# Kernel tuning notes

Hardware: AMD Instinct MI355X
Metric: run time of the kernel (lower is better)

The kernel has to match this reference:

```python
import jax, jax.numpy as jnp
import numpy as np

B, C_IN, C_OUT, H, W, K, NK = 16, 256, 256, 64, 64, 3, 2
EPS = 1e-8


def setup_inputs() -> dict:
    key = jax.random.key(0)
    k1, k2, k3, k4 = jax.random.split(key, 4)
    x = jax.random.normal(k1, (B, C_IN, H, W), dtype=jnp.float32)
    mod = jax.random.normal(k2, (B, C_IN), dtype=jnp.float32)
    kernel_mod = jax.random.normal(k3, (B, NK), dtype=jnp.float32)
    # kernel bank: [num_conv_kernels, dim_out, dim_in, k, k] (kaiming-ish scale)
    weights = jax.random.normal(k4, (NK, C_OUT, C_IN, K, K), dtype=jnp.float32) / np.sqrt(C_IN * K * K)
    gamma = jnp.ones((C_OUT,), dtype=jnp.float32)
    return {"x": x, "mod": mod, "kernel_mod": kernel_mod, "weights": weights, "gamma": gamma}


def _block(x, mod, kernel_mod, weights, gamma):
    # adaptive kernel selection: softmax-mix the kernel bank per sample
    attn = jax.nn.softmax(kernel_mod, axis=-1)                       # [b, n]
    w = jnp.einsum('bn,noikl->boikl', attn, weights)                 # [b, o, i, k, k]
    # style modulation over input channels
    w = w * (mod[:, None, :, None, None] + 1.0)
    # demodulation
    denom = jnp.clip(jnp.sum(w * w, axis=(2, 3, 4), keepdims=True), EPS)
    w = w * jax.lax.rsqrt(denom)
    # per-sample conv (groups=b trick in torch) -> vmap over batch
    def conv_one(fmap, wb):
        return jax.lax.conv_general_dilated(
            fmap[None], wb, window_strides=(1, 1), padding='SAME',
            dimension_numbers=('NCHW', 'OIHW', 'NCHW'))[0]
    y = jax.vmap(conv_one)(x, w)                                     # [b, o, h, w]
    # RMSNorm over channel dim: F.normalize(x, dim=1) * gamma * sqrt(dim)
    norm = jnp.sqrt(jnp.sum(y * y, axis=1, keepdims=True))
    y = y / jnp.maximum(norm, 1e-12)
    y = y * gamma[None, :, None, None] * (gamma.shape[0] ** 0.5)
    # SiLU
    return y * jax.nn.sigmoid(y)


def reference(x, mod, kernel_mod, weights, gamma):
    return _block(x, mod, kernel_mod, weights, gamma)
```

## Files before the change

### kernel.cpp

```cpp
#include <hip/hip_runtime.h>
#include <math.h>


typedef __attribute__((ext_vector_type(8))) short short8;
typedef __attribute__((ext_vector_type(4))) float f32x4;

#define GLL16(src, dst)                                                       \
  __builtin_amdgcn_global_load_lds(                                           \
      (const __attribute__((address_space(1))) unsigned int*)(src),           \
      (__attribute__((address_space(3))) unsigned int*)(dst), 16, 0, 0)

static __device__ __forceinline__ unsigned short f2bf(float v) {
  union { float f; unsigned u; } u;
  u.f = v;
  unsigned r = u.u + 0x7FFF + ((u.u >> 16) & 1);
  return (unsigned short)(r >> 16);
}

__global__ __launch_bounds__(256) void wprep(
    const float* __restrict__ mod, const float* __restrict__ kmod,
    const float* __restrict__ weights, unsigned short* __restrict__ wq) {
  int blk = blockIdx.x;
  int b = blk >> 5, oq = blk & 31;
  int t = threadIdx.x;
  int o_l = t >> 5, its = t & 31;
  int o = oq * 8 + o_l;

  float k0 = kmod[b * 2 + 0], k1 = kmod[b * 2 + 1];
  float mx = fmaxf(k0, k1);
  float e0 = expf(k0 - mx), e1 = expf(k1 - mx);
  float ai = 1.0f / (e0 + e1);
  float a0 = e0 * ai, a1 = e1 * ai;

  float wv[9][8];
  float s = 0.0f;
  const float* w0 = &weights[((size_t)o * 256 + its * 8) * 9];
  const float* w1 = w0 + 589824;
#pragma unroll
  for (int e = 0; e < 8; ++e) {
    float f = mod[b * 256 + its * 8 + e] + 1.0f;
#pragma unroll
    for (int j = 0; j < 9; ++j) {
      float v = (a0 * w0[e * 9 + j] + a1 * w1[e * 9 + j]) * f;
      wv[j][e] = v;
      s = fmaf(v, v, s);
    }
  }

  __shared__ float red[8][32];
  __shared__ float scl[8];
  red[o_l][its] = s;
  __syncthreads();
  if (t < 8) {
    float tot = 0.0f;
#pragma unroll
    for (int k = 0; k < 32; ++k) tot += red[t][k];
    scl[t] = rsqrtf(fmaxf(tot, 1e-8f));
  }
  __syncthreads();
  float sc = scl[o_l];

  int c = its >> 1, io = its & 1;
  int ot = o >> 7, mf = (o & 127) >> 4, lm = o & 15;
  size_t cbase = ((size_t)(b * 32 + ot * 16 + c)) * 20480;
#pragma unroll
  for (int j = 0; j < 9; ++j) {
    int p = io * 10 + j;
    int sp = p >> 2, g = p & 3;
    short8 pk;
#pragma unroll
    for (int e = 0; e < 8; ++e) pk[e] = (short)f2bf(wv[j][e] * sc);
    *(short8*)(wq + cbase + sp * 4096 + mf * 512 + g * 128 + lm * 8) = pk;
  }
  {
    int c2 = t >> 4, io2 = (t >> 3) & 1, olq = t & 7;
    int o2 = oq * 8 + olq;
    int ot2 = o2 >> 7, mf2 = (o2 & 127) >> 4, lm2 = o2 & 15;
    int p2 = io2 * 10 + 9;
    int sp2 = p2 >> 2, g2 = p2 & 3;
    short8 z = {0, 0, 0, 0, 0, 0, 0, 0};
    *(short8*)(wq + ((size_t)(b * 32 + ot2 * 16 + c2)) * 20480 + sp2 * 4096 +
               mf2 * 512 + g2 * 128 + lm2 * 8) = z;
  }
}

__global__ __launch_bounds__(256) void xprep(
    const float* __restrict__ x, unsigned short* __restrict__ xq) {
  int blk = blockIdx.x;
  int rowp = blk % 66;
  int bc = blk / 66;
  int b = bc >> 4, c = bc & 15;
  int t = threadIdx.x;
  size_t obase = (size_t)blk * 1056;

  if (rowp == 0 || rowp == 65) {
    for (int idx = t; idx < 1056; idx += 256) xq[obase + idx] = 0;
    return;
  }
  __shared__ __align__(16) unsigned short xs2[1056];
  int row = rowp - 1;
  for (int idx = t; idx < 1056; idx += 256) xs2[idx] = 0;
  __syncthreads();
#pragma unroll
  for (int k = 0; k < 4; ++k) {
    int idx = t + k * 256;
    int il = idx >> 6, col = idx & 63;
    float v = x[(((size_t)b * 256 + c * 16 + il) * 64 + row) * 64 + col];
    xs2[(col + 1) * 16 + il] = f2bf(v);
  }
  __syncthreads();
  if (t < 132) {
    int S = 4 * (rowp & 7) + t;
    int fl = ((S >> 3) & 1) | (((S >> 4) & 1) << 1);
    *(short8*)(xq + obase + (size_t)(t ^ fl) * 8) = *(const short8*)&xs2[t * 8];
  }
}

__global__ __launch_bounds__(256, 1) void conv_mfma(
    const unsigned short* __restrict__ xq, const unsigned short* __restrict__ wq,
    float* __restrict__ out) {
  __shared__ __align__(16) unsigned short wsm[2][20480];
  __shared__ __align__(16) unsigned short xsm[2][10560];

  int bid = blockIdx.x;
  int xcd = bid & 7;
  int kk = bid >> 3;
  int b = xcd * 2 + (kk >> 4);
  int rem = kk & 15;
  int ot = rem >> 3;
  int rt = rem & 7;
  int r0 = rt * 8;

  int t = threadIdx.x;
  int w = t >> 6, lane = t & 63;
  int g = (t >> 4) & 3, lm = t & 15;
  int aoff = lane * 16;

  int b0_[5], b1_[5];
#pragma unroll
  for (int s = 0; s < 5; ++s) {
    int p = 4 * s + g;
    int io = (p >= 10) ? 1 : 0;
    int j = p - 10 * io;
    int jd3, jm3;
    if (j == 9) { jd3 = 0; jm3 = 0; }
    else { jd3 = (j >= 3) + (j >= 6); jm3 = j - 3 * jd3; }
    int la0 = ((2 * w + jd3) * 66 + lm + jm3) * 32 + io * 16;
    la0 ^= (((la0 >> 7) & 1) << 4) ^ (((la0 >> 8) & 1) << 5);
    b0_[s] = la0;
    int la1 = ((2 * w + 1 + jd3) * 66 + lm + jm3) * 32 + io * 16;
    la1 ^= (((la1 >> 7) & 1) << 4) ^ (((la1 >> 8) & 1) << 5);
    b1_[s] = la1;
  }

  f32x4 acc[8][8];
#pragma unroll
  for (int mf = 0; mf < 8; ++mf)
#pragma unroll
    for (int nf = 0; nf < 8; ++nf) acc[mf][nf] = (f32x4){0.f, 0.f, 0.f, 0.f};

#define WGLL(cn, nb, r)                                                         \
  {                                                                             \
    const unsigned short* s_ =                                                  \
        wq + ((size_t)(b * 32 + ot * 16 + (cn))) * 20480 + ((r) * 256 + t) * 8; \
    GLL16(s_, &wsm[nb][((r) * 256 + t) * 8]);                                   \
  }
#define XGLL(cn, nb, r)                                                          \
  {                                                                              \
    const unsigned short* s_ =                                                   \
        xq + ((size_t)((b * 16 + (cn)) * 66 + r0)) * 1056 + ((r) * 256 + t) * 8; \
    GLL16(s_, &xsm[nb][((r) * 256 + t) * 8]);                                    \
  }
#define XGLLP(cn, nb)                                                            \
  {                                                                              \
    const unsigned short* s_ =                                                   \
        xq + ((size_t)((b * 16 + (cn)) * 66 + r0)) * 1056 + (1280 + t) * 8;      \
    GLL16(s_, &xsm[nb][(1280 + t) * 8]);                                         \
  }

#define LGKM0 asm volatile("s_waitcnt lgkmcnt(0)" ::: "memory")
#define VM0 asm volatile("s_waitcnt vmcnt(0)" ::: "memory")

  WGLL(0, 0, 0); WGLL(0, 0, 1); WGLL(0, 0, 2); WGLL(0, 0, 3); WGLL(0, 0, 4);
  WGLL(0, 0, 5); WGLL(0, 0, 6); WGLL(0, 0, 7); WGLL(0, 0, 8); WGLL(0, 0, 9);
  XGLL(0, 0, 0); XGLL(0, 0, 1); XGLL(0, 0, 2); XGLL(0, 0, 3); XGLL(0, 0, 4);
  if (t < 40) XGLLP(0, 0);
  VM0;
  __builtin_amdgcn_s_barrier();

  for (int c = 0; c < 16; ++c) {
    int cur = c & 1;
    const char* wsb = (const char*)wsm[cur] + aoff;
    const char* xsb = (const char*)xsm[cur];
#pragma unroll
    for (int s = 0; s < 5; ++s) {
      if (c < 15) {
        int nb = cur ^ 1;
        if (s == 0) { WGLL(c + 1, nb, 0); WGLL(c + 1, nb, 1); WGLL(c + 1, nb, 2); }
        if (s == 1) { WGLL(c + 1, nb, 3); WGLL(c + 1, nb, 4); WGLL(c + 1, nb, 5); }
        if (s == 2) { WGLL(c + 1, nb, 6); WGLL(c + 1, nb, 7); WGLL(c + 1, nb, 8); }
        if (s == 3) {
          WGLL(c + 1, nb, 9);
          XGLL(c + 1, nb, 0); XGLL(c + 1, nb, 1); XGLL(c + 1, nb, 2);
          XGLL(c + 1, nb, 3); XGLL(c + 1, nb, 4);
          if (t < 40) XGLLP(c + 1, nb);
        }
      }
      short8 A[8], Bv[8];
#pragma unroll
      for (int mf = 0; mf < 8; ++mf)
        A[mf] = *(const short8*)(wsb + s * 8192 + mf * 1024);
#pragma unroll
      for (int nc = 0; nc < 4; ++nc) {
        Bv[nc] = *(const short8*)(xsb + b0_[s] + nc * 512);
        Bv[4 + nc] = *(const short8*)(xsb + b1_[s] + nc * 512);
      }
      __builtin_amdgcn_s_setprio(1);
#pragma unroll
      for (int nf = 0; nf < 8; ++nf)
#pragma unroll
        for (int mf = 0; mf < 8; ++mf)
          acc[mf][nf] = __builtin_amdgcn_mfma_f32_16x16x32_bf16(
              A[mf], Bv[nf], acc[mf][nf], 0, 0, 0);
      __builtin_amdgcn_s_setprio(0);
    }
    LGKM0;
    VM0;
    __builtin_amdgcn_s_barrier();
  }

#pragma unroll
  for (int mf = 0; mf < 8; ++mf)
#pragma unroll
    for (int nf = 0; nf < 8; ++nf) {
      int row = r0 + 2 * w + (nf >> 2);
      int col = (nf & 3) * 16 + lm;
#pragma unroll
      for (int q = 0; q < 4; ++q) {
        int o = ot * 128 + mf * 16 + g * 4 + q;
        out[(((size_t)b * 256 + o) * 64 + row) * 64 + col] = acc[mf][nf][q];
      }
    }
#undef WGLL
#undef XGLL
#undef XGLLP
#undef LGKM0
#undef VM0
}

__global__ __launch_bounds__(256) void norm_kernel(
    float* __restrict__ y, const float* __restrict__ gamma) {
  int blk = blockIdx.x;
  int b = blk >> 6, h = blk & 63;
  int t = threadIdx.x;
  int p = t & 63, og = t >> 6;

  size_t base = (((size_t)b * 256) * 64 + h) * 64 + p;
  float yv[64];
  float s = 0.0f;
#pragma unroll
  for (int k = 0; k < 64; k++) {
    yv[k] = y[base + (size_t)(og * 64 + k) * 4096];
    s = fmaf(yv[k], yv[k], s);
  }

  __shared__ float red[4][64];
  __shared__ float invs[64];
  red[og][p] = s;
  __syncthreads();
  if (og == 0) {
    float tot = red[0][p] + red[1][p] + red[2][p] + red[3][p];
    float nrm = sqrtf(tot);
    invs[p] = 16.0f / fmaxf(nrm, 1e-12f);
  }
  __syncthreads();
  float iv = invs[p];
#pragma unroll
  for (int k = 0; k < 64; k++) {
    int o = og * 64 + k;
    float v = yv[k] * iv * gamma[o];
    float sg = 1.0f / (1.0f + expf(-v));
    y[base + (size_t)o * 4096] = v * sg;
  }
}

extern "C" void kernel_launch(void* const* d_in, const int* in_sizes, int n_in,
                              void* d_out, int out_size, void* d_ws, size_t ws_size,
                              hipStream_t stream) {
  const float* x = (const float*)d_in[0];
  const float* mod = (const float*)d_in[1];
  const float* kmod = (const float*)d_in[2];
  const float* weights = (const float*)d_in[3];
  const float* gamma = (const float*)d_in[4];
  float* out = (float*)d_out;

  unsigned short* wq = (unsigned short*)d_ws;
  unsigned short* xq = (unsigned short*)((char*)d_ws + 20987904);

  wprep<<<512, 256, 0, stream>>>(mod, kmod, weights, wq);
  xprep<<<16 * 16 * 66, 256, 0, stream>>>(x, xq);
  conv_mfma<<<256, 256, 0, stream>>>(xq, wq, out);
  norm_kernel<<<16 * 64, 256, 0, stream>>>(out, gamma);
}
```

Baseline: 136.9 us.

## Fuse RMSNorm and SiLU into conv kernel with full-channel tiles and 32x32 MFMA

Each conv block now computes all 256 output channels for four rows, so the channel-dim RMS norm and SiLU can be applied in-register before the single store. This removes the separate norm kernel and its extra read/write pass over the fp32 output. The MFMA shape moves from 16x16x32 to 32x32x16, the weight/input layouts and the split-phase pipelined prefetch schedule are reworked to match, and the LDS swizzle is dropped. The larger weight tile per block raises LDS use and register pressure, and the unswizzled layout may cause bank conflicts.

```diff
diff --git a/kernel.cpp b/kernel.cpp
--- a/kernel.cpp
+++ b/kernel.cpp
@@ -3,7 +3,7 @@
 
 
 typedef __attribute__((ext_vector_type(8))) short short8;
-typedef __attribute__((ext_vector_type(4))) float f32x4;
+typedef __attribute__((ext_vector_type(16))) float f32x16;
 
 #define GLL16(src, dst)                                                       \
   __builtin_amdgcn_global_load_lds(                                           \
@@ -61,26 +61,15 @@
   float sc = scl[o_l];
 
   int c = its >> 1, io = its & 1;
-  int ot = o >> 7, mf = (o & 127) >> 4, lm = o & 15;
-  size_t cbase = ((size_t)(b * 32 + ot * 16 + c)) * 20480;
+  int oh = o >> 7, mf = (o >> 5) & 3;
+  int lane2 = (o & 31) + io * 32;
+  size_t cbase = ((size_t)(b * 16 + c)) * 36864 + oh * 2048 + mf * 512 + lane2 * 8;
 #pragma unroll
   for (int j = 0; j < 9; ++j) {
-    int p = io * 10 + j;
-    int sp = p >> 2, g = p & 3;
     short8 pk;
 #pragma unroll
     for (int e = 0; e < 8; ++e) pk[e] = (short)f2bf(wv[j][e] * sc);
-    *(short8*)(wq + cbase + sp * 4096 + mf * 512 + g * 128 + lm * 8) = pk;
-  }
-  {
-    int c2 = t >> 4, io2 = (t >> 3) & 1, olq = t & 7;
-    int o2 = oq * 8 + olq;
-    int ot2 = o2 >> 7, mf2 = (o2 & 127) >> 4, lm2 = o2 & 15;
-    int p2 = io2 * 10 + 9;
-    int sp2 = p2 >> 2, g2 = p2 & 3;
-    short8 z = {0, 0, 0, 0, 0, 0, 0, 0};
-    *(short8*)(wq + ((size_t)(b * 32 + ot2 * 16 + c2)) * 20480 + sp2 * 4096 +
-               mf2 * 512 + g2 * 128 + lm2 * 8) = z;
+    *(short8*)(wq + cbase + j * 4096) = pk;
   }
 }
 
@@ -109,179 +98,193 @@
     xs2[(col + 1) * 16 + il] = f2bf(v);
   }
   __syncthreads();
-  if (t < 132) {
-    int S = 4 * (rowp & 7) + t;
-    int fl = ((S >> 3) & 1) | (((S >> 4) & 1) << 1);
-    *(short8*)(xq + obase + (size_t)(t ^ fl) * 8) = *(const short8*)&xs2[t * 8];
-  }
-}
-
-__global__ __launch_bounds__(256, 1) void conv_mfma(
+  if (t < 132) *(short8*)(xq + obase + (size_t)t * 8) = *(const short8*)&xs2[t * 8];
+}
+
+__global__ __launch_bounds__(256, 1) void conv_fused(
     const unsigned short* __restrict__ xq, const unsigned short* __restrict__ wq,
-    float* __restrict__ out) {
-  __shared__ __align__(16) unsigned short wsm[2][20480];
-  __shared__ __align__(16) unsigned short xsm[2][10560];
+    const float* __restrict__ gamma, float* __restrict__ out) {
+  __shared__ __align__(16) unsigned short wsm[36864];
+  __shared__ __align__(16) unsigned short xsm[2][8192];
+  __shared__ float redl[1024];
+  __shared__ float invs[256];
+  __shared__ float gsm[256];
 
   int bid = blockIdx.x;
   int xcd = bid & 7;
   int kk = bid >> 3;
   int b = xcd * 2 + (kk >> 4);
-  int rem = kk & 15;
-  int ot = rem >> 3;
-  int rt = rem & 7;
-  int r0 = rt * 8;
+  int rt = kk & 15;
+  int r0 = rt * 4;
 
   int t = threadIdx.x;
   int w = t >> 6, lane = t & 63;
-  int g = (t >> 4) & 3, lm = t & 15;
-  int aoff = lane * 16;
-
-  int b0_[5], b1_[5];
-#pragma unroll
-  for (int s = 0; s < 5; ++s) {
-    int p = 4 * s + g;
-    int io = (p >= 10) ? 1 : 0;
-    int j = p - 10 * io;
-    int jd3, jm3;
-    if (j == 9) { jd3 = 0; jm3 = 0; }
-    else { jd3 = (j >= 3) + (j >= 6); jm3 = j - 3 * jd3; }
-    int la0 = ((2 * w + jd3) * 66 + lm + jm3) * 32 + io * 16;
-    la0 ^= (((la0 >> 7) & 1) << 4) ^ (((la0 >> 8) & 1) << 5);
-    b0_[s] = la0;
-    int la1 = ((2 * w + 1 + jd3) * 66 + lm + jm3) * 32 + io * 16;
-    la1 ^= (((la1 >> 7) & 1) << 4) ^ (((la1 >> 8) & 1) << 5);
-    b1_[s] = la1;
-  }
-
-  f32x4 acc[8][8];
-#pragma unroll
-  for (int mf = 0; mf < 8; ++mf)
-#pragma unroll
-    for (int nf = 0; nf < 8; ++nf) acc[mf][nf] = (f32x4){0.f, 0.f, 0.f, 0.f};
-
-#define WGLL(cn, nb, r)                                                         \
-  {                                                                             \
-    const unsigned short* s_ =                                                  \
-        wq + ((size_t)(b * 32 + ot * 16 + (cn))) * 20480 + ((r) * 256 + t) * 8; \
-    GLL16(s_, &wsm[nb][((r) * 256 + t) * 8]);                                   \
-  }
-#define XGLL(cn, nb, r)                                                          \
-  {                                                                              \
-    const unsigned short* s_ =                                                   \
-        xq + ((size_t)((b * 16 + (cn)) * 66 + r0)) * 1056 + ((r) * 256 + t) * 8; \
-    GLL16(s_, &xsm[nb][((r) * 256 + t) * 8]);                                    \
-  }
-#define XGLLP(cn, nb)                                                            \
-  {                                                                              \
-    const unsigned short* s_ =                                                   \
-        xq + ((size_t)((b * 16 + (cn)) * 66 + r0)) * 1056 + (1280 + t) * 8;      \
-    GLL16(s_, &xsm[nb][(1280 + t) * 8]);                                         \
-  }
-
+  int oh = w >> 1, pq = w & 1;
+  int l31 = lane & 31, l5 = lane >> 5;
+
+  gsm[t] = gamma[t];
+
+  const char* aw = (const char*)wsm + oh * 4096 + lane * 16;
+  const char* xb0 = (const char*)xsm[0] + ((2 * pq) * 66 + l31) * 32 + l5 * 16;
+  const char* xb1 = (const char*)xsm[1] + ((2 * pq) * 66 + l31) * 32 + l5 * 16;
+
+  f32x16 acc[4][4];
+#pragma unroll
+  for (int mf = 0; mf < 4; ++mf)
+#pragma unroll
+    for (int nf = 0; nf < 4; ++nf)
+#pragma unroll
+      for (int q = 0; q < 16; ++q) acc[mf][nf][q] = 0.f;
+
+#define GLLL(cn)                                                               \
+  _Pragma("unroll") for (int r = 0; r < 8; ++r) {                              \
+    GLL16(wq + ((size_t)(b * 16 + (cn))) * 36864 + (r * 256 + t) * 8,          \
+          &wsm[(r * 256 + t) * 8]);                                            \
+  }
+#define GLLH(cn)                                                               \
+  _Pragma("unroll") for (int r = 0; r < 10; ++r) {                             \
+    GLL16(wq + ((size_t)(b * 16 + (cn))) * 36864 + 16384 + (r * 256 + t) * 8,  \
+          &wsm[16384 + (r * 256 + t) * 8]);                                    \
+  }
+#define GLLX(cn, nb)                                                           \
+  _Pragma("unroll") for (int r = 0; r < 4; ++r) {                              \
+    GLL16(xq + ((size_t)((b * 16 + (cn)) * 66 + r0)) * 1056 + (r * 256 + t) * 8, \
+          &xsm[nb][(r * 256 + t) * 8]);                                        \
+  }
+
+  short8 PA[4], PB[4], QA[4], QB[4];
+
+#define DSRD(SA, SB, TAP, XB)                                                  \
+  {                                                                            \
+    _Pragma("unroll") for (int mf = 0; mf < 4; ++mf)                           \
+        SA[mf] = *(const short8*)(aw + (TAP) * 8192 + mf * 1024);              \
+    const char* xb_ = (XB) ? xb1 : xb0;                                        \
+    _Pragma("unroll") for (int r = 0; r < 2; ++r)                              \
+        _Pragma("unroll") for (int h = 0; h < 2; ++h)                          \
+            SB[r * 2 + h] = *(const short8*)(xb_ + ((TAP) / 3) * 2112 +        \
+                                             ((TAP) % 3) * 32 + r * 2112 +     \
+                                             h * 1024);                        \
+  }
+
+#define MFMAT(SA, SB)                                                          \
+  {                                                                            \
+    _Pragma("unroll") for (int nf = 0; nf < 4; ++nf)                           \
+        _Pragma("unroll") for (int mf = 0; mf < 4; ++mf)                       \
+            acc[mf][nf] = __builtin_amdgcn_mfma_f32_32x32x16_bf16(             \
+                SA[mf], SB[nf], acc[mf][nf], 0, 0, 0);                         \
+  }
+
+#define SBAR __builtin_amdgcn_sched_barrier(0)
 #define LGKM0 asm volatile("s_waitcnt lgkmcnt(0)" ::: "memory")
-#define VM0 asm volatile("s_waitcnt vmcnt(0)" ::: "memory")
-
-  WGLL(0, 0, 0); WGLL(0, 0, 1); WGLL(0, 0, 2); WGLL(0, 0, 3); WGLL(0, 0, 4);
-  WGLL(0, 0, 5); WGLL(0, 0, 6); WGLL(0, 0, 7); WGLL(0, 0, 8); WGLL(0, 0, 9);
-  XGLL(0, 0, 0); XGLL(0, 0, 1); XGLL(0, 0, 2); XGLL(0, 0, 3); XGLL(0, 0, 4);
-  if (t < 40) XGLLP(0, 0);
-  VM0;
-  __builtin_amdgcn_s_barrier();
-
-  for (int c = 0; c < 16; ++c) {
-    int cur = c & 1;
-    const char* wsb = (const char*)wsm[cur] + aoff;
-    const char* xsb = (const char*)xsm[cur];
-#pragma unroll
-    for (int s = 0; s < 5; ++s) {
-      if (c < 15) {
-        int nb = cur ^ 1;
-        if (s == 0) { WGLL(c + 1, nb, 0); WGLL(c + 1, nb, 1); WGLL(c + 1, nb, 2); }
-        if (s == 1) { WGLL(c + 1, nb, 3); WGLL(c + 1, nb, 4); WGLL(c + 1, nb, 5); }
-        if (s == 2) { WGLL(c + 1, nb, 6); WGLL(c + 1, nb, 7); WGLL(c + 1, nb, 8); }
-        if (s == 3) {
-          WGLL(c + 1, nb, 9);
-          XGLL(c + 1, nb, 0); XGLL(c + 1, nb, 1); XGLL(c + 1, nb, 2);
-          XGLL(c + 1, nb, 3); XGLL(c + 1, nb, 4);
-          if (t < 40) XGLLP(c + 1, nb);
+#define VMC(n) asm volatile("s_waitcnt vmcnt(" #n ")" ::: "memory")
+#define BAR __builtin_amdgcn_s_barrier()
+
+#define CBODY(R0A, R0B, R1A, R1B, C, XB)                                       \
+  {                                                                            \
+    DSRD(R1A, R1B, 1, XB); SBAR; MFMAT(R0A, R0B);                    \
+    DSRD(R0A, R0B, 2, XB); SBAR; MFMAT(R1A, R1B);                    \
+    DSRD(R1A, R1B, 3, XB); SBAR; MFMAT(R0A, R0B);                    \
+    LGKM0; SBAR;                                                               \
+    BAR;                                              \
+    GLLL((C) + 1); GLLX((C) + 1, (XB) ^ 1);                                    \
+    VMC(12); SBAR;                                            \
+    DSRD(R0A, R0B, 4, XB); SBAR; MFMAT(R1A, R1B);                    \
+    DSRD(R1A, R1B, 5, XB); SBAR; MFMAT(R0A, R0B);                    \
+    DSRD(R0A, R0B, 6, XB); SBAR; MFMAT(R1A, R1B);                    \
+    DSRD(R1A, R1B, 7, XB); SBAR; MFMAT(R0A, R0B);                    \
+    DSRD(R0A, R0B, 8, XB); SBAR; MFMAT(R1A, R1B);                    \
+    LGKM0; SBAR;                                                               \
+    BAR;                                              \
+    GLLH((C) + 1);                                                             \
+    VMC(10); SBAR;                                   \
+    DSRD(R1A, R1B, 0, (XB) ^ 1); SBAR; MFMAT(R0A, R0B);              \
+  }
+
+#define CTAIL(R0A, R0B, R1A, R1B, XB)                                          \
+  {                                                                            \
+    DSRD(R1A, R1B, 1, XB); SBAR; MFMAT(R0A, R0B);                              \
+    DSRD(R0A, R0B, 2, XB); SBAR; MFMAT(R1A, R1B);                              \
+    DSRD(R1A, R1B, 3, XB); SBAR; MFMAT(R0A, R0B);                              \
+    DSRD(R0A, R0B, 4, XB); SBAR; MFMAT(R1A, R1B);                              \
+    DSRD(R1A, R1B, 5, XB); SBAR; MFMAT(R0A, R0B);                              \
+    DSRD(R0A, R0B, 6, XB); SBAR; MFMAT(R1A, R1B);                              \
+    DSRD(R1A, R1B, 7, XB); SBAR; MFMAT(R0A, R0B);                              \
+    DSRD(R0A, R0B, 8, XB); SBAR; MFMAT(R1A, R1B);                              \
+    MFMAT(R0A, R0B);                                                           \
+  }
+
+  GLLL(0); GLLH(0); GLLX(0, 0);
+  VMC(0);
+  BAR;
+  SBAR;
+  DSRD(PA, PB, 0, 0);
+  SBAR;
+
+  for (int cc = 0; cc < 16; cc += 2) {
+    CBODY(PA, PB, QA, QB, cc, 0);
+    if (cc < 14) {
+      CBODY(QA, QB, PA, PB, cc + 1, 1);
+    } else {
+      CTAIL(QA, QB, PA, PB, 1);
+    }
+  }
+
+#pragma unroll
+  for (int r = 0; r < 2; ++r)
+#pragma unroll
+    for (int h = 0; h < 2; ++h) {
+      int nf = r * 2 + h;
+      float ps = 0.f;
+#pragma unroll
+      for (int mf = 0; mf < 4; ++mf)
+#pragma unroll
+        for (int q = 0; q < 16; ++q) {
+          float v = acc[mf][nf][q];
+          ps = fmaf(v, v, ps);
         }
-      }
-      short8 A[8], Bv[8];
-#pragma unroll
-      for (int mf = 0; mf < 8; ++mf)
-        A[mf] = *(const short8*)(wsb + s * 8192 + mf * 1024);
-#pragma unroll
-      for (int nc = 0; nc < 4; ++nc) {
-        Bv[nc] = *(const short8*)(xsb + b0_[s] + nc * 512);
-        Bv[4 + nc] = *(const short8*)(xsb + b1_[s] + nc * 512);
-      }
-      __builtin_amdgcn_s_setprio(1);
-#pragma unroll
-      for (int nf = 0; nf < 8; ++nf)
-#pragma unroll
-        for (int mf = 0; mf < 8; ++mf)
-          acc[mf][nf] = __builtin_amdgcn_mfma_f32_16x16x32_bf16(
-              A[mf], Bv[nf], acc[mf][nf], 0, 0, 0);
-      __builtin_amdgcn_s_setprio(0);
+      int px = (2 * pq + r) * 64 + h * 32 + l31;
+      redl[(oh * 2 + l5) * 256 + px] = ps;
     }
-    LGKM0;
-    VM0;
-    __builtin_amdgcn_s_barrier();
-  }
-
-#pragma unroll
-  for (int mf = 0; mf < 8; ++mf)
-#pragma unroll
-    for (int nf = 0; nf < 8; ++nf) {
-      int row = r0 + 2 * w + (nf >> 2);
-      int col = (nf & 3) * 16 + lm;
-#pragma unroll
-      for (int q = 0; q < 4; ++q) {
-        int o = ot * 128 + mf * 16 + g * 4 + q;
-        out[(((size_t)b * 256 + o) * 64 + row) * 64 + col] = acc[mf][nf][q];
-      }
+  __syncthreads();
+  {
+    float ssum = redl[t] + redl[256 + t] + redl[512 + t] + redl[768 + t];
+    invs[t] = 16.0f / fmaxf(sqrtf(ssum), 1e-12f);
+  }
+  __syncthreads();
+  float iv4[4];
+#pragma unroll
+  for (int r = 0; r < 2; ++r)
+#pragma unroll
+    for (int h = 0; h < 2; ++h)
+      iv4[r * 2 + h] = invs[(2 * pq + r) * 64 + h * 32 + l31];
+
+#pragma unroll
+  for (int mf = 0; mf < 4; ++mf)
+#pragma unroll
+    for (int q = 0; q < 16; ++q) {
+      int o = oh * 128 + mf * 32 + (q & 3) + 8 * (q >> 2) + 4 * l5;
+      float g = gsm[o];
+      size_t ob = (((size_t)b * 256 + o) * 64);
+#pragma unroll
+      for (int r = 0; r < 2; ++r)
+#pragma unroll
+        for (int h = 0; h < 2; ++h) {
+          float v = acc[mf][r * 2 + h][q] * iv4[r * 2 + h] * g;
+          float sg = 1.0f / (1.0f + expf(-v));
+          out[(ob + (r0 + 2 * pq + r)) * 64 + h * 32 + l31] = v * sg;
+        }
     }
-#undef WGLL
-#undef XGLL
-#undef XGLLP
+#undef GLLL
+#undef GLLH
+#undef GLLX
+#undef DSRD
+#undef MFMAT
+#undef SBAR
 #undef LGKM0
-#undef VM0
-}
-
-__global__ __launch_bounds__(256) void norm_kernel(
-    float* __restrict__ y, const float* __restrict__ gamma) {
-  int blk = blockIdx.x;
-  int b = blk >> 6, h = blk & 63;
-  int t = threadIdx.x;
-  int p = t & 63, og = t >> 6;
-
-  size_t base = (((size_t)b * 256) * 64 + h) * 64 + p;
-  float yv[64];
-  float s = 0.0f;
-#pragma unroll
-  for (int k = 0; k < 64; k++) {
-    yv[k] = y[base + (size_t)(og * 64 + k) * 4096];
-    s = fmaf(yv[k], yv[k], s);
-  }
-
-  __shared__ float red[4][64];
-  __shared__ float invs[64];
-  red[og][p] = s;
-  __syncthreads();
-  if (og == 0) {
-    float tot = red[0][p] + red[1][p] + red[2][p] + red[3][p];
-    float nrm = sqrtf(tot);
-    invs[p] = 16.0f / fmaxf(nrm, 1e-12f);
-  }
-  __syncthreads();
-  float iv = invs[p];
-#pragma unroll
-  for (int k = 0; k < 64; k++) {
-    int o = og * 64 + k;
-    float v = yv[k] * iv * gamma[o];
-    float sg = 1.0f / (1.0f + expf(-v));
-    y[base + (size_t)o * 4096] = v * sg;
-  }
+#undef VMC
+#undef BAR
+#undef CBODY
+#undef CTAIL
 }
 
 extern "C" void kernel_launch(void* const* d_in, const int* in_sizes, int n_in,
@@ -294,11 +297,10 @@
   const float* gamma = (const float*)d_in[4];
   float* out = (float*)d_out;
 
-  unsigned short* wq = (unsigned short*)d_ws;
-  unsigned short* xq = (unsigned short*)((char*)d_ws + 20987904);
+  unsigned short* xq = (unsigned short*)d_ws;
+  unsigned short* wq = (unsigned short*)((char*)d_ws + 35684352);
 
   wprep<<<512, 256, 0, stream>>>(mod, kmod, weights, wq);
   xprep<<<16 * 16 * 66, 256, 0, stream>>>(x, xq);
-  conv_mfma<<<256, 256, 0, stream>>>(xq, wq, out);
-  norm_kernel<<<16 * 64, 256, 0, stream>>>(out, gamma);
-}
+  conv_fused<<<256, 256, 0, stream>>>(xq, wq, gamma, out);
+}
```

Measured after the change: 269.3 us. 96.7% more time.
